# Kernel tuning notes

Measured on AMD Instinct MI355X. Metric: run time of the kernel, lower is better.

Reference implementation:

```python
import jax, jax.numpy as jnp
import numpy as np

C = 128   # recurrent/value channels
CK = 64   # key channels

def conv1x1(x, W, b):
    # x: [B,Cin,H,W], W: [Cout,Cin], b: [Cout]
    return jnp.einsum('bchw,oc->bohw', x, W) + b[None, :, None, None]

def extract_windows(x):
    # zero-padded 3x3 windows, matching F.unfold(kernel=3, padding=1)
    # x: [B,C,H2,W2] -> [B,C,9,H2,W2], tap order = (ky, kx) row-major
    B, c, H2, W2 = x.shape
    xp = jnp.pad(x, ((0, 0), (0, 0), (1, 1), (1, 1)))
    taps = [xp[:, :, dy:dy + H2, dx:dx + W2] for dy in range(3) for dx in range(3)]
    return jnp.stack(taps, axis=2)

def setup_inputs() -> dict:
    key = jax.random.key(0)
    ks = jax.random.split(key, 12)
    B, H, W = 2, 256, 512
    H2, W2 = 128, 256
    s = 0.02
    return {
        'h_prev': jax.random.normal(ks[0], (B, C, H2, W2), jnp.float32),
        'h_init': jax.random.normal(ks[1], (B, C, H, W), jnp.float32),
        'Wq':   jax.random.normal(ks[2], (CK, C), jnp.float32) * s,
        'bq':   jnp.zeros((CK,), jnp.float32),
        'Wk':   jax.random.normal(ks[3], (CK, C), jnp.float32) * s,
        'bk':   jnp.zeros((CK,), jnp.float32),
        'Wvp':  jax.random.normal(ks[4], (C, C), jnp.float32) * s,
        'bvp':  jnp.zeros((C,), jnp.float32),
        'Wvi':  jax.random.normal(ks[5], (C, C), jnp.float32) * s,
        'bvi':  jnp.zeros((C,), jnp.float32),
        'Wout': jax.random.normal(ks[6], (C, C), jnp.float32) * s,
        'bout': jnp.zeros((C,), jnp.float32),
    }

def reference(h_prev, h_init, Wq, bq, Wk, bk, Wvp, bvp, Wvi, bvi, Wout, bout):
    B, _, H, W = h_init.shape
    _, _, H2, W2 = h_prev.shape
    ry, rx = H // H2, W // W2

    q = conv1x1(h_init, Wq, bq)        # [B,CK,H,W]
    k = conv1x1(h_prev, Wk, bk)        # [B,CK,H2,W2]
    v = conv1x1(h_prev, Wvp, bvp)      # [B,C,H2,W2]

    k_win = extract_windows(k)         # [B,CK,9,H2,W2]
    v_win = extract_windows(v)         # [B,C,9,H2,W2]

    # q at fine res, grouped by coarse cell (nearest-neighbor broadcast of k/v)
    q_r = q.transpose(0, 2, 3, 1).reshape(B, H2, ry, W2, rx, CK)  # [B,H2,ry,W2,rx,CK]
    # scores over 9 window taps (zero-padded taps give score 0, as in unfold)
    scores = jnp.einsum('byaxdc,bcjyx->byaxdj', q_r, k_win)       # [B,H2,ry,W2,rx,9]
    a = jax.nn.softmax(scores, axis=-1)
    x = jnp.einsum('byaxdj,bcjyx->bcyaxd', a, v_win)              # [B,C,H2,ry,W2,rx]
    x = x.reshape(B, C, H, W)

    v_init = conv1x1(h_init, Wvi, bvi)
    return conv1x1(v_init + x, Wout, bout)
```

## Files before the change

### kernel.cpp

```cpp
#include <hip/hip_runtime.h>
#include <cstdint>
#include <cstddef>

#define THREADS 256
#define FTHREADS 512

typedef __attribute__((ext_vector_type(8))) short short8;
typedef __attribute__((ext_vector_type(4))) float f32x4;

#define MFMA(a, b, c) __builtin_amdgcn_mfma_f32_16x16x32_bf16((a), (b), (c), 0, 0, 0)

static constexpr int kC    = 128;
static constexpr int kImgC = 128 * 256;
static constexpr int kImgF = 256 * 512;

__device__ __forceinline__ unsigned short f2bf(float f) {
  unsigned u = __builtin_bit_cast(unsigned, f);
  u += 0x7fffu + ((u >> 16) & 1u);
  return (unsigned short)(u >> 16);
}
__device__ __forceinline__ unsigned pack_bf16(float lo, float hi) {
  return (unsigned)f2bf(lo) | ((unsigned)f2bf(hi) << 16);
}
__device__ __forceinline__ float bf_up(unsigned short u) {
  return __builtin_bit_cast(float, (unsigned)u << 16);
}

__device__ __forceinline__ void stage_tile(char* lds, const float* __restrict__ src,
                                           size_t cstride, int tid) {
  const int l = tid & 63, w = tid >> 6;
  const int pxl = l & 7;
  const int cg  = l >> 3;
  #pragma unroll
  for (int i = 0; i < 16; ++i) {
    const int px = pxl + 8 * (i & 7);
    const int c  = 2 * (cg + 8 * (w + 4 * (i >> 3)));
    float f0 = src[(size_t)c * cstride + px];
    float f1 = src[(size_t)(c + 1) * cstride + px];
    const int chunk = (c >> 3) ^ (px & 7);
    *(unsigned*)(lds + px * 256 + chunk * 16 + (c & 7) * 2) = pack_bf16(f0, f1);
  }
}

__device__ __forceinline__ short8 ldA(const char* lds, int mt, int kt, int l) {
  const int px = mt * 16 + (l & 15);
  const int chunk = (kt * 4 + (l >> 4)) ^ (px & 7);
  return *(const short8*)(lds + px * 256 + chunk * 16);
}

__global__ __launch_bounds__(THREADS) void cast_w(
    const float* __restrict__ Wq, const float* __restrict__ Wk,
    const float* __restrict__ Wvp, const float* __restrict__ Wvi,
    const float* __restrict__ Wout, unsigned short* __restrict__ dst) {
  int i = blockIdx.x * THREADS + threadIdx.x;
  float v;
  if (i < 8192)       v = Wq[i];
  else if (i < 16384) v = Wk[i - 8192];
  else if (i < 32768) v = Wvp[i - 16384];
  else if (i < 49152) v = Wvi[i - 32768];
  else                v = Wout[i - 49152];
  dst[i] = f2bf(v);
}

__global__ __launch_bounds__(THREADS, 4) void coarse_kv(
    const float* __restrict__ h_prev, const unsigned short* __restrict__ wbuf,
    const float* __restrict__ bk, const float* __restrict__ bvp,
    float* __restrict__ kbuf, float* __restrict__ vbuf) {
  __shared__ char xs[16384];
  const int tid = threadIdx.x;
  const int l = tid & 63, w = tid >> 6;
  const int m = l & 15, g = l >> 4;
  const int chq = w * 16 + m;

  const int tile = blockIdx.x;
  const int b    = tile >> 9;
  const int p0   = (tile & 511) * 64;
  const int p0g  = tile * 64;

  const short8* wkp = (const short8*)(wbuf + 8192);
  const short8* wvp = (const short8*)(wbuf + 16384);
  short8 fk[4], fv[2][4];
  #pragma unroll
  for (int kt = 0; kt < 4; ++kt) fk[kt] = wkp[chq * 16 + kt * 4 + g];
  #pragma unroll
  for (int nt = 0; nt < 2; ++nt)
    #pragma unroll
    for (int kt = 0; kt < 4; ++kt)
      fv[nt][kt] = wvp[(nt * 64 + chq) * 16 + kt * 4 + g];

  stage_tile(xs, h_prev + (size_t)b * kC * kImgC + p0, kImgC, tid);
  __syncthreads();

  {
    const float bl = bk[chq];
    #pragma unroll
    for (int mt = 0; mt < 4; ++mt) {
      f32x4 acc = {bl, bl, bl, bl};
      #pragma unroll
      for (int kt = 0; kt < 4; ++kt) acc = MFMA(ldA(xs, mt, kt, l), fk[kt], acc);
      #pragma unroll
      for (int r = 0; r < 4; ++r)
        kbuf[(size_t)(p0g + mt * 16 + g * 4 + r) * 64 + chq] = acc[r];
    }
  }
  #pragma unroll
  for (int nt = 0; nt < 2; ++nt) {
    const float bl = bvp[nt * 64 + chq];
    #pragma unroll
    for (int mt = 0; mt < 4; ++mt) {
      f32x4 acc = {bl, bl, bl, bl};
      #pragma unroll
      for (int kt = 0; kt < 4; ++kt) acc = MFMA(ldA(xs, mt, kt, l), fv[nt][kt], acc);
      #pragma unroll
      for (int r = 0; r < 4; ++r)
        vbuf[(size_t)(p0g + mt * 16 + g * 4 + r) * 128 + nt * 64 + chq] = acc[r];
    }
  }
}

__global__ __launch_bounds__(FTHREADS, 2) void fine_fused(
    const float* __restrict__ h_init, const unsigned short* __restrict__ wbuf,
    const float* __restrict__ bq, const float* __restrict__ bvi,
    const float* __restrict__ bout,
    const float* __restrict__ kbuf, const float* __restrict__ vbuf,
    float* __restrict__ out) {
  __shared__ char xs[32768];
  __shared__ unsigned short qs[128 * 72];
  __shared__ float ks_[102 * 76];
  __shared__ float vs_[102 * 140];

  const int tid = threadIdx.x;
  const int l = tid & 63, w = tid >> 6;
  const int m = l & 15, g = l >> 4;

  const int bid = blockIdx.x;
  const int b   = bid >> 10;
  const int r10 = bid & 1023;
  const int y2  = r10 >> 3;
  const int x0  = (r10 & 7) * 64;
  const int x20 = x0 >> 1;

  const size_t fbase = (size_t)b * kC * kImgF;
  const float* kb = kbuf + (size_t)b * kImgC * 64;
  const float* vb = vbuf + (size_t)b * kImgC * 128;

  const short8* wqp = (const short8*)wbuf;
  const short8* wip = (const short8*)(wbuf + 32768);
  const short8* wop = (const short8*)(wbuf + 49152);

  if (tid < 256)
    stage_tile(xs, h_init + fbase + (size_t)(2 * y2) * 512 + x0, kImgF, tid);
  else
    stage_tile(xs + 16384, h_init + fbase + (size_t)(2 * y2 + 1) * 512 + x0, kImgF, tid - 256);

  #pragma unroll
  for (int it = 0; it < 7; ++it) {
    const int i = tid + it * 512;
    if (i < 3264) {
      const int cy = i / 1088;
      const int rem = i - cy * 1088;
      const int cx = rem >> 5, cp = rem & 31;
      const int yy = y2 + cy - 1, xx = x20 + cx - 1;
      float2 kv = make_float2(0.f, 0.f);
      if (yy >= 0 && yy < 128 && xx >= 0 && xx < 256)
        kv = *(const float2*)(kb + ((size_t)yy * 256 + xx) * 64 + 2 * cp);
      *(float2*)(ks_ + (cy * 34 + cx) * 76 + 2 * cp) = kv;
    }
  }
  #pragma unroll
  for (int it = 0; it < 13; ++it) {
    const int i = tid + it * 512;
    if (i < 6528) {
      const int cy = i / 2176;
      const int rem = i - cy * 2176;
      const int cx = rem >> 6, cp = rem & 63;
      const int yy = y2 + cy - 1, xx = x20 + cx - 1;
      float2 vv = make_float2(0.f, 0.f);
      if (yy >= 0 && yy < 128 && xx >= 0 && xx < 256)
        vv = *(const float2*)(vb + ((size_t)yy * 256 + xx) * 128 + 2 * cp);
      *(float2*)(vs_ + (cy * 34 + cx) * 140 + 2 * cp) = vv;
    }
  }
  __syncthreads();

  const int chq4 = (w & 3) * 16 + m;
  const int hh   = w >> 2;
  {
    short8 fq[4];
    #pragma unroll
    for (int kt = 0; kt < 4; ++kt) fq[kt] = wqp[chq4 * 16 + kt * 4 + g];
    const float bl = bq[chq4];
    #pragma unroll
    for (int mt = 0; mt < 4; ++mt) {
      f32x4 acc = {bl, bl, bl, bl};
      #pragma unroll
      for (int kt = 0; kt < 4; ++kt) acc = MFMA(ldA(xs, hh * 4 + mt, kt, l), fq[kt], acc);
      #pragma unroll
      for (int r = 0; r < 4; ++r)
        qs[(hh * 64 + mt * 16 + g * 4 + r) * 72 + chq4] = f2bf(acc[r]);
    }
  }

  const int ch = w * 16 + m;
  f32x4 vacc[8];
  {
    short8 fi[4];
    #pragma unroll
    for (int kt = 0; kt < 4; ++kt) fi[kt] = wip[ch * 16 + kt * 4 + g];
    const float bl = bvi[ch];
    #pragma unroll
    for (int mt = 0; mt < 8; ++mt) {
      f32x4 acc = {bl, bl, bl, bl};
      #pragma unroll
      for (int kt = 0; kt < 4; ++kt) acc = MFMA(ldA(xs, mt, kt, l), fi[kt], acc);
      vacc[mt] = acc;
    }
  }
  __syncthreads();

  #pragma unroll
  for (int mt = 0; mt < 8; ++mt) {
    #pragma unroll
    for (int r = 0; r < 4; ++r) {
      const int px = mt * 16 + g * 4 + r;
      const int chunk = (ch >> 3) ^ (px & 7);
      *(unsigned short*)(xs + px * 256 + chunk * 16 + (ch & 7) * 2) = f2bf(vacc[mt][r]);
    }
  }
  __syncthreads();

  {
    const int apx = tid >> 2;
    const int sub = tid & 3;
    const int cc  = ((apx & 63) >> 1) + 1;

    float qf[16];
    {
      const uint4* qp = (const uint4*)((const char*)qs + apx * 144 + sub * 32);
      const uint4 u0 = qp[0], u1 = qp[1];
      const unsigned uu[8] = {u0.x, u0.y, u0.z, u0.w, u1.x, u1.y, u1.z, u1.w};
      #pragma unroll
      for (int i = 0; i < 8; ++i) {
        qf[2 * i]     = __builtin_bit_cast(float, uu[i] << 16);
        qf[2 * i + 1] = __builtin_bit_cast(float, uu[i] & 0xffff0000u);
      }
    }

    float a[9];
    #pragma unroll
    for (int j = 0; j < 9; ++j) {
      const int cell = (j / 3) * 34 + cc + (j % 3) - 1;
      const float4* kp = (const float4*)(ks_ + cell * 76 + sub * 16);
      const float4 k0 = kp[0], k1 = kp[1], k2 = kp[2], k3 = kp[3];
      float s = qf[0]*k0.x + qf[1]*k0.y + qf[2]*k0.z + qf[3]*k0.w
              + qf[4]*k1.x + qf[5]*k1.y + qf[6]*k1.z + qf[7]*k1.w
              + qf[8]*k2.x + qf[9]*k2.y + qf[10]*k2.z + qf[11]*k2.w
              + qf[12]*k3.x + qf[13]*k3.y + qf[14]*k3.z + qf[15]*k3.w;
      s += __shfl_xor(s, 1);
      s += __shfl_xor(s, 2);
      a[j] = s;
    }
    float mx = a[0];
    #pragma unroll
    for (int j = 1; j < 9; ++j) mx = fmaxf(mx, a[j]);
    float den = 0.f;
    #pragma unroll
    for (int j = 0; j < 9; ++j) { a[j] = __expf(a[j] - mx); den += a[j]; }
    const float inv = 1.f / den;

    float tt[32];
    #pragma unroll
    for (int i = 0; i < 32; ++i) tt[i] = 0.f;
    #pragma unroll
    for (int j = 0; j < 9; ++j) {
      const int cell = (j / 3) * 34 + cc + (j % 3) - 1;
      const float aj = a[j] * inv;
      const float4* vp = (const float4*)(vs_ + cell * 140 + sub * 32);
      const float4 v0 = vp[0], v1 = vp[1], v2 = vp[2], v3 = vp[3];
      const float4 v4 = vp[4], v5 = vp[5], v6 = vp[6], v7 = vp[7];
      tt[0]+=aj*v0.x;  tt[1]+=aj*v0.y;  tt[2]+=aj*v0.z;  tt[3]+=aj*v0.w;
      tt[4]+=aj*v1.x;  tt[5]+=aj*v1.y;  tt[6]+=aj*v1.z;  tt[7]+=aj*v1.w;
      tt[8]+=aj*v2.x;  tt[9]+=aj*v2.y;  tt[10]+=aj*v2.z; tt[11]+=aj*v2.w;
      tt[12]+=aj*v3.x; tt[13]+=aj*v3.y; tt[14]+=aj*v3.z; tt[15]+=aj*v3.w;
      tt[16]+=aj*v4.x; tt[17]+=aj*v4.y; tt[18]+=aj*v4.z; tt[19]+=aj*v4.w;
      tt[20]+=aj*v5.x; tt[21]+=aj*v5.y; tt[22]+=aj*v5.z; tt[23]+=aj*v5.w;
      tt[24]+=aj*v6.x; tt[25]+=aj*v6.y; tt[26]+=aj*v6.z; tt[27]+=aj*v6.w;
      tt[28]+=aj*v7.x; tt[29]+=aj*v7.y; tt[30]+=aj*v7.z; tt[31]+=aj*v7.w;
    }
    #pragma unroll
    for (int i = 0; i < 16; ++i) {
      const int c2 = sub * 32 + 2 * i;
      const int chunk = (c2 >> 3) ^ (apx & 7);
      unsigned* p = (unsigned*)(xs + apx * 256 + chunk * 16 + (c2 & 7) * 2);
      const unsigned u = *p;
      const float lo = bf_up((unsigned short)u) + tt[2 * i];
      const float hi = bf_up((unsigned short)(u >> 16)) + tt[2 * i + 1];
      *p = pack_bf16(lo, hi);
    }
  }
  __syncthreads();

  {
    short8 fo[4];
    #pragma unroll
    for (int kt = 0; kt < 4; ++kt) fo[kt] = wop[ch * 16 + kt * 4 + g];
    const float bl = bout[ch];
    #pragma unroll
    for (int mt = 0; mt < 8; ++mt) {
      f32x4 acc = {bl, bl, bl, bl};
      #pragma unroll
      for (int kt = 0; kt < 4; ++kt) acc = MFMA(ldA(xs, mt, kt, l), fo[kt], acc);
      const int px = mt * 16 + g * 4;
      *(float4*)(out + fbase + (size_t)ch * kImgF
                 + (size_t)(2 * y2 + (px >> 6)) * 512 + x0 + (px & 63)) =
          make_float4(acc[0], acc[1], acc[2], acc[3]);
    }
  }
}

extern "C" void kernel_launch(void* const* d_in, const int* in_sizes, int n_in,
                              void* d_out, int out_size, void* d_ws, size_t ws_size,
                              hipStream_t stream) {
  const float* h_prev = (const float*)d_in[0];
  const float* h_init = (const float*)d_in[1];
  const float* Wq   = (const float*)d_in[2];
  const float* bq   = (const float*)d_in[3];
  const float* Wk   = (const float*)d_in[4];
  const float* bk   = (const float*)d_in[5];
  const float* Wvp  = (const float*)d_in[6];
  const float* bvp  = (const float*)d_in[7];
  const float* Wvi  = (const float*)d_in[8];
  const float* bvi  = (const float*)d_in[9];
  const float* Wout = (const float*)d_in[10];
  const float* bout = (const float*)d_in[11];
  float* out = (float*)d_out;

  char* ws = (char*)d_ws;
  unsigned short* wbuf = (unsigned short*)ws;
  float* kbuf = (float*)(ws + 131072);
  float* vbuf = (float*)(ws + 131072 + (size_t)65536 * 64 * 4);

  cast_w<<<256, THREADS, 0, stream>>>(Wq, Wk, Wvp, Wvi, Wout, wbuf);
  coarse_kv<<<1024, THREADS, 0, stream>>>(h_prev, wbuf, bk, bvp, kbuf, vbuf);
  fine_fused<<<2048, FTHREADS, 0, stream>>>(h_init, wbuf, bq, bvi, bout,
                                            kbuf, vbuf, out);
}
```

Before: 394.1 us.

## Fuse coarse K/V projection into fine kernel, recomputing halo per block

Removes the separate coarse_kv kernel and its fp32 K/V workspace round-trip. Each fine block now loads the 3x34 coarse halo of h_prev, projects it to K and V with MFMA directly into shared memory, and zeroes out-of-bounds cells. The h_init tile is prefetched into registers before this work and written to LDS afterwards, so the global loads overlap the halo projection. The cost is redundant K/V computation, since each coarse cell is recomputed by several neighbouring blocks, plus higher register pressure from holding 32 prefetched floats per thread.

Result: slower. 436.3 us (+10.7%).

```diff
diff --git a/kernel.cpp b/kernel.cpp
--- a/kernel.cpp
+++ b/kernel.cpp
@@ -24,22 +24,6 @@
 }
 __device__ __forceinline__ float bf_up(unsigned short u) {
   return __builtin_bit_cast(float, (unsigned)u << 16);
-}
-
-__device__ __forceinline__ void stage_tile(char* lds, const float* __restrict__ src,
-                                           size_t cstride, int tid) {
-  const int l = tid & 63, w = tid >> 6;
-  const int pxl = l & 7;
-  const int cg  = l >> 3;
-  #pragma unroll
-  for (int i = 0; i < 16; ++i) {
-    const int px = pxl + 8 * (i & 7);
-    const int c  = 2 * (cg + 8 * (w + 4 * (i >> 3)));
-    float f0 = src[(size_t)c * cstride + px];
-    float f1 = src[(size_t)(c + 1) * cstride + px];
-    const int chunk = (c >> 3) ^ (px & 7);
-    *(unsigned*)(lds + px * 256 + chunk * 16 + (c & 7) * 2) = pack_bf16(f0, f1);
-  }
 }
 
 __device__ __forceinline__ short8 ldA(const char* lds, int mt, int kt, int l) {
@@ -62,68 +46,12 @@
   dst[i] = f2bf(v);
 }
 
-__global__ __launch_bounds__(THREADS, 4) void coarse_kv(
-    const float* __restrict__ h_prev, const unsigned short* __restrict__ wbuf,
-    const float* __restrict__ bk, const float* __restrict__ bvp,
-    float* __restrict__ kbuf, float* __restrict__ vbuf) {
-  __shared__ char xs[16384];
-  const int tid = threadIdx.x;
-  const int l = tid & 63, w = tid >> 6;
-  const int m = l & 15, g = l >> 4;
-  const int chq = w * 16 + m;
-
-  const int tile = blockIdx.x;
-  const int b    = tile >> 9;
-  const int p0   = (tile & 511) * 64;
-  const int p0g  = tile * 64;
-
-  const short8* wkp = (const short8*)(wbuf + 8192);
-  const short8* wvp = (const short8*)(wbuf + 16384);
-  short8 fk[4], fv[2][4];
-  #pragma unroll
-  for (int kt = 0; kt < 4; ++kt) fk[kt] = wkp[chq * 16 + kt * 4 + g];
-  #pragma unroll
-  for (int nt = 0; nt < 2; ++nt)
-    #pragma unroll
-    for (int kt = 0; kt < 4; ++kt)
-      fv[nt][kt] = wvp[(nt * 64 + chq) * 16 + kt * 4 + g];
-
-  stage_tile(xs, h_prev + (size_t)b * kC * kImgC + p0, kImgC, tid);
-  __syncthreads();
-
-  {
-    const float bl = bk[chq];
-    #pragma unroll
-    for (int mt = 0; mt < 4; ++mt) {
-      f32x4 acc = {bl, bl, bl, bl};
-      #pragma unroll
-      for (int kt = 0; kt < 4; ++kt) acc = MFMA(ldA(xs, mt, kt, l), fk[kt], acc);
-      #pragma unroll
-      for (int r = 0; r < 4; ++r)
-        kbuf[(size_t)(p0g + mt * 16 + g * 4 + r) * 64 + chq] = acc[r];
-    }
-  }
-  #pragma unroll
-  for (int nt = 0; nt < 2; ++nt) {
-    const float bl = bvp[nt * 64 + chq];
-    #pragma unroll
-    for (int mt = 0; mt < 4; ++mt) {
-      f32x4 acc = {bl, bl, bl, bl};
-      #pragma unroll
-      for (int kt = 0; kt < 4; ++kt) acc = MFMA(ldA(xs, mt, kt, l), fv[nt][kt], acc);
-      #pragma unroll
-      for (int r = 0; r < 4; ++r)
-        vbuf[(size_t)(p0g + mt * 16 + g * 4 + r) * 128 + nt * 64 + chq] = acc[r];
-    }
-  }
-}
-
 __global__ __launch_bounds__(FTHREADS, 2) void fine_fused(
-    const float* __restrict__ h_init, const unsigned short* __restrict__ wbuf,
-    const float* __restrict__ bq, const float* __restrict__ bvi,
-    const float* __restrict__ bout,
-    const float* __restrict__ kbuf, const float* __restrict__ vbuf,
-    float* __restrict__ out) {
+    const float* __restrict__ h_prev, const float* __restrict__ h_init,
+    const unsigned short* __restrict__ wbuf,
+    const float* __restrict__ bq, const float* __restrict__ bk,
+    const float* __restrict__ bvp, const float* __restrict__ bvi,
+    const float* __restrict__ bout, float* __restrict__ out) {
   __shared__ char xs[32768];
   __shared__ unsigned short qs[128 * 72];
   __shared__ float ks_[102 * 76];
@@ -141,44 +69,83 @@
   const int x20 = x0 >> 1;
 
   const size_t fbase = (size_t)b * kC * kImgF;
-  const float* kb = kbuf + (size_t)b * kImgC * 64;
-  const float* vb = vbuf + (size_t)b * kImgC * 128;
 
   const short8* wqp = (const short8*)wbuf;
+  const short8* wkp = (const short8*)(wbuf + 8192);
+  const short8* wvp = (const short8*)(wbuf + 16384);
   const short8* wip = (const short8*)(wbuf + 32768);
   const short8* wop = (const short8*)(wbuf + 49152);
 
-  if (tid < 256)
-    stage_tile(xs, h_init + fbase + (size_t)(2 * y2) * 512 + x0, kImgF, tid);
-  else
-    stage_tile(xs + 16384, h_init + fbase + (size_t)(2 * y2 + 1) * 512 + x0, kImgF, tid - 256);
-
+  const int tl = tid & 255;
+  const int sl = tl & 63, sw = tl >> 6;
+  const int spxl = sl & 7, scg = sl >> 3;
+  const float* xsrc = h_init + fbase + (size_t)(2 * y2 + (tid >> 8)) * 512 + x0;
+  float xf0[16], xf1[16];
   #pragma unroll
-  for (int it = 0; it < 7; ++it) {
-    const int i = tid + it * 512;
-    if (i < 3264) {
-      const int cy = i / 1088;
-      const int rem = i - cy * 1088;
-      const int cx = rem >> 5, cp = rem & 31;
+  for (int i = 0; i < 16; ++i) {
+    const int px = spxl + 8 * (i & 7);
+    const int c  = 2 * (scg + 8 * (sw + 4 * (i >> 3)));
+    xf0[i] = xsrc[(size_t)c * kImgF + px];
+    xf1[i] = xsrc[(size_t)(c + 1) * kImgF + px];
+  }
+
+  {
+    const float* hp = h_prev + (size_t)b * kC * kImgC;
+    const int pxl = l & 7, cg8 = l >> 3;
+    const int c = 2 * (cg8 + 8 * w);
+    #pragma unroll
+    for (int t = 0; t < 13; ++t) {
+      const int p = pxl + 8 * t;
+      const int cy = p / 34, cx = p - cy * 34;
       const int yy = y2 + cy - 1, xx = x20 + cx - 1;
-      float2 kv = make_float2(0.f, 0.f);
-      if (yy >= 0 && yy < 128 && xx >= 0 && xx < 256)
-        kv = *(const float2*)(kb + ((size_t)yy * 256 + xx) * 64 + 2 * cp);
-      *(float2*)(ks_ + (cy * 34 + cx) * 76 + 2 * cp) = kv;
-    }
-  }
-  #pragma unroll
-  for (int it = 0; it < 13; ++it) {
-    const int i = tid + it * 512;
-    if (i < 6528) {
-      const int cy = i / 2176;
-      const int rem = i - cy * 2176;
-      const int cx = rem >> 6, cp = rem & 63;
-      const int yy = y2 + cy - 1, xx = x20 + cx - 1;
-      float2 vv = make_float2(0.f, 0.f);
-      if (yy >= 0 && yy < 128 && xx >= 0 && xx < 256)
-        vv = *(const float2*)(vb + ((size_t)yy * 256 + xx) * 128 + 2 * cp);
-      *(float2*)(vs_ + (cy * 34 + cx) * 140 + 2 * cp) = vv;
+      float f0 = 0.f, f1 = 0.f;
+      if (p < 102 && (unsigned)yy < 128u && (unsigned)xx < 256u) {
+        const size_t pos = (size_t)yy * 256 + xx;
+        f0 = hp[(size_t)c * kImgC + pos];
+        f1 = hp[(size_t)(c + 1) * kImgC + pos];
+      }
+      if (p < 102) {
+        const int chunk = (c >> 3) ^ (p & 7);
+        *(unsigned*)(xs + p * 256 + chunk * 16 + (c & 7) * 2) = pack_bf16(f0, f1);
+      }
+    }
+  }
+  __syncthreads();
+
+  for (int j = w; j < 84; j += 8) {
+    const int mt = j / 12, cg12 = j - mt * 12;
+    const bool isk = cg12 < 4;
+    const int och = (isk ? cg12 : cg12 - 4) * 16 + m;
+    const short8* wp = isk ? wkp : wvp;
+    const float bl = isk ? bk[och] : bvp[och];
+    f32x4 acc = {bl, bl, bl, bl};
+    #pragma unroll
+    for (int kt = 0; kt < 4; ++kt)
+      acc = MFMA(ldA(xs, mt, kt, l), wp[och * 16 + kt * 4 + g], acc);
+    #pragma unroll
+    for (int r = 0; r < 4; ++r) {
+      const int cell = mt * 16 + g * 4 + r;
+      if (cell < 102) {
+        const int cy = cell / 34, cx = cell - cy * 34;
+        const int yy = y2 + cy - 1, xx = x20 + cx - 1;
+        const float val =
+            ((unsigned)yy < 128u && (unsigned)xx < 256u) ? acc[r] : 0.f;
+        if (isk) ks_[cell * 76 + och] = val;
+        else     vs_[cell * 140 + och] = val;
+      }
+    }
+  }
+  __syncthreads();
+
+  {
+    char* dst = xs + (tid >> 8) * 16384;
+    #pragma unroll
+    for (int i = 0; i < 16; ++i) {
+      const int px = spxl + 8 * (i & 7);
+      const int c  = 2 * (scg + 8 * (sw + 4 * (i >> 3)));
+      const int chunk = (c >> 3) ^ (px & 7);
+      *(unsigned*)(dst + px * 256 + chunk * 16 + (c & 7) * 2) =
+          pack_bf16(xf0[i], xf1[i]);
     }
   }
   __syncthreads();
@@ -337,11 +304,8 @@
 
   char* ws = (char*)d_ws;
   unsigned short* wbuf = (unsigned short*)ws;
-  float* kbuf = (float*)(ws + 131072);
-  float* vbuf = (float*)(ws + 131072 + (size_t)65536 * 64 * 4);
 
   cast_w<<<256, THREADS, 0, stream>>>(Wq, Wk, Wvp, Wvi, Wout, wbuf);
-  coarse_kv<<<1024, THREADS, 0, stream>>>(h_prev, wbuf, bk, bvp, kbuf, vbuf);
-  fine_fused<<<2048, FTHREADS, 0, stream>>>(h_init, wbuf, bq, bvi, bout,
-                                            kbuf, vbuf, out);
-}
+  fine_fused<<<2048, FTHREADS, 0, stream>>>(h_prev, h_init, wbuf,
+                                            bq, bk, bvp, bvi, bout, out);
+}
```

## Store K/V in bf16 and tile fine kernel as 8x16 2D blocks

Applied to the files above, without the earlier changes.

Coarse K and V intermediates are now written as bf16 instead of fp32, halving their global traffic and LDS footprint. The fine kernel switches from 2-row by 64-column tiles to 8-row by 16-column tiles, so the coarse halo shrinks from 3x34 cells to 6x10 cells per block, which cuts redundant K/V staging. Smaller LDS use allows launch bounds of 4 blocks per CU. The tradeoffs are extra bf16 rounding of K/V and narrower 64-byte row segments in global loads and stores.

Measured after the change: 369.0 us. -6.4%, faster.

```diff
diff --git a/kernel.cpp b/kernel.cpp
--- a/kernel.cpp
+++ b/kernel.cpp
@@ -25,21 +25,11 @@
 __device__ __forceinline__ float bf_up(unsigned short u) {
   return __builtin_bit_cast(float, (unsigned)u << 16);
 }
-
-__device__ __forceinline__ void stage_tile(char* lds, const float* __restrict__ src,
-                                           size_t cstride, int tid) {
-  const int l = tid & 63, w = tid >> 6;
-  const int pxl = l & 7;
-  const int cg  = l >> 3;
-  #pragma unroll
-  for (int i = 0; i < 16; ++i) {
-    const int px = pxl + 8 * (i & 7);
-    const int c  = 2 * (cg + 8 * (w + 4 * (i >> 3)));
-    float f0 = src[(size_t)c * cstride + px];
-    float f1 = src[(size_t)(c + 1) * cstride + px];
-    const int chunk = (c >> 3) ^ (px & 7);
-    *(unsigned*)(lds + px * 256 + chunk * 16 + (c & 7) * 2) = pack_bf16(f0, f1);
-  }
+__device__ __forceinline__ float bf_lo(unsigned u) {
+  return __builtin_bit_cast(float, u << 16);
+}
+__device__ __forceinline__ float bf_hi(unsigned u) {
+  return __builtin_bit_cast(float, u & 0xffff0000u);
 }
 
 __device__ __forceinline__ short8 ldA(const char* lds, int mt, int kt, int l) {
@@ -65,7 +55,7 @@
 __global__ __launch_bounds__(THREADS, 4) void coarse_kv(
     const float* __restrict__ h_prev, const unsigned short* __restrict__ wbuf,
     const float* __restrict__ bk, const float* __restrict__ bvp,
-    float* __restrict__ kbuf, float* __restrict__ vbuf) {
+    unsigned short* __restrict__ kbuf, unsigned short* __restrict__ vbuf) {
   __shared__ char xs[16384];
   const int tid = threadIdx.x;
   const int l = tid & 63, w = tid >> 6;
@@ -88,7 +78,19 @@
     for (int kt = 0; kt < 4; ++kt)
       fv[nt][kt] = wvp[(nt * 64 + chq) * 16 + kt * 4 + g];
 
-  stage_tile(xs, h_prev + (size_t)b * kC * kImgC + p0, kImgC, tid);
+  {
+    const float* src = h_prev + (size_t)b * kC * kImgC + p0;
+    const int pxl = l & 7, cg = l >> 3;
+    #pragma unroll
+    for (int i = 0; i < 16; ++i) {
+      const int px = pxl + 8 * (i & 7);
+      const int c  = 2 * (cg + 8 * (w + 4 * (i >> 3)));
+      float f0 = src[(size_t)c * kImgC + px];
+      float f1 = src[(size_t)(c + 1) * kImgC + px];
+      const int chunk = (c >> 3) ^ (px & 7);
+      *(unsigned*)(xs + px * 256 + chunk * 16 + (c & 7) * 2) = pack_bf16(f0, f1);
+    }
+  }
   __syncthreads();
 
   {
@@ -100,7 +102,7 @@
       for (int kt = 0; kt < 4; ++kt) acc = MFMA(ldA(xs, mt, kt, l), fk[kt], acc);
       #pragma unroll
       for (int r = 0; r < 4; ++r)
-        kbuf[(size_t)(p0g + mt * 16 + g * 4 + r) * 64 + chq] = acc[r];
+        kbuf[(size_t)(p0g + mt * 16 + g * 4 + r) * 64 + chq] = f2bf(acc[r]);
     }
   }
   #pragma unroll
@@ -113,21 +115,21 @@
       for (int kt = 0; kt < 4; ++kt) acc = MFMA(ldA(xs, mt, kt, l), fv[nt][kt], acc);
       #pragma unroll
       for (int r = 0; r < 4; ++r)
-        vbuf[(size_t)(p0g + mt * 16 + g * 4 + r) * 128 + nt * 64 + chq] = acc[r];
-    }
-  }
-}
-
-__global__ __launch_bounds__(FTHREADS, 2) void fine_fused(
+        vbuf[(size_t)(p0g + mt * 16 + g * 4 + r) * 128 + nt * 64 + chq] = f2bf(acc[r]);
+    }
+  }
+}
+
+__global__ __launch_bounds__(FTHREADS, 4) void fine_fused(
     const float* __restrict__ h_init, const unsigned short* __restrict__ wbuf,
     const float* __restrict__ bq, const float* __restrict__ bvi,
     const float* __restrict__ bout,
-    const float* __restrict__ kbuf, const float* __restrict__ vbuf,
+    const unsigned short* __restrict__ kbuf, const unsigned short* __restrict__ vbuf,
     float* __restrict__ out) {
   __shared__ char xs[32768];
   __shared__ unsigned short qs[128 * 72];
-  __shared__ float ks_[102 * 76];
-  __shared__ float vs_[102 * 140];
+  __shared__ unsigned short ks_[60 * 80];
+  __shared__ unsigned short vs_[60 * 144];
 
   const int tid = threadIdx.x;
   const int l = tid & 63, w = tid >> 6;
@@ -136,49 +138,63 @@
   const int bid = blockIdx.x;
   const int b   = bid >> 10;
   const int r10 = bid & 1023;
-  const int y2  = r10 >> 3;
-  const int x0  = (r10 & 7) * 64;
+  const int ty  = r10 >> 5;
+  const int tx  = r10 & 31;
+  const int y0  = ty * 8;
+  const int x0  = tx * 16;
+  const int y20 = y0 >> 1;
   const int x20 = x0 >> 1;
 
   const size_t fbase = (size_t)b * kC * kImgF;
-  const float* kb = kbuf + (size_t)b * kImgC * 64;
-  const float* vb = vbuf + (size_t)b * kImgC * 128;
+  const unsigned short* kb = kbuf + (size_t)b * kImgC * 64;
+  const unsigned short* vb = vbuf + (size_t)b * kImgC * 128;
 
   const short8* wqp = (const short8*)wbuf;
   const short8* wip = (const short8*)(wbuf + 32768);
   const short8* wop = (const short8*)(wbuf + 49152);
 
-  if (tid < 256)
-    stage_tile(xs, h_init + fbase + (size_t)(2 * y2) * 512 + x0, kImgF, tid);
-  else
-    stage_tile(xs + 16384, h_init + fbase + (size_t)(2 * y2 + 1) * 512 + x0, kImgF, tid - 256);
-
-  #pragma unroll
-  for (int it = 0; it < 7; ++it) {
+  {
+    const int half = tid >> 8;
+    const int tl = tid & 255;
+    const int sl = tl & 63, sw = tl >> 6;
+    const int pxl = sl & 7, cg = sl >> 3;
+    #pragma unroll
+    for (int i = 0; i < 16; ++i) {
+      const int px = half * 64 + pxl + 8 * (i & 7);
+      const int row = px >> 4, col = px & 15;
+      const int c  = 2 * (cg + 8 * (sw + 4 * (i >> 3)));
+      const size_t off = (size_t)(y0 + row) * 512 + x0 + col;
+      float f0 = h_init[fbase + (size_t)c * kImgF + off];
+      float f1 = h_init[fbase + (size_t)(c + 1) * kImgF + off];
+      const int chunk = (c >> 3) ^ (px & 7);
+      *(unsigned*)(xs + px * 256 + chunk * 16 + (c & 7) * 2) = pack_bf16(f0, f1);
+    }
+  }
+
+  #pragma unroll
+  for (int it = 0; it < 2; ++it) {
     const int i = tid + it * 512;
-    if (i < 3264) {
-      const int cy = i / 1088;
-      const int rem = i - cy * 1088;
-      const int cx = rem >> 5, cp = rem & 31;
-      const int yy = y2 + cy - 1, xx = x20 + cx - 1;
-      float2 kv = make_float2(0.f, 0.f);
-      if (yy >= 0 && yy < 128 && xx >= 0 && xx < 256)
-        kv = *(const float2*)(kb + ((size_t)yy * 256 + xx) * 64 + 2 * cp);
-      *(float2*)(ks_ + (cy * 34 + cx) * 76 + 2 * cp) = kv;
-    }
-  }
-  #pragma unroll
-  for (int it = 0; it < 13; ++it) {
+    if (i < 960) {
+      const int cell = i >> 4, cp = i & 15;
+      const int cy = cell / 10, cx = cell - cy * 10;
+      const int yy = y20 + cy - 1, xx = x20 + cx - 1;
+      uint2 val = make_uint2(0u, 0u);
+      if ((unsigned)yy < 128u && (unsigned)xx < 256u)
+        val = *(const uint2*)(kb + ((size_t)yy * 256 + xx) * 64 + cp * 4);
+      *(uint2*)((char*)ks_ + cell * 160 + (cp >> 2) * 40 + (cp & 3) * 8) = val;
+    }
+  }
+  #pragma unroll
+  for (int it = 0; it < 4; ++it) {
     const int i = tid + it * 512;
-    if (i < 6528) {
-      const int cy = i / 2176;
-      const int rem = i - cy * 2176;
-      const int cx = rem >> 6, cp = rem & 63;
-      const int yy = y2 + cy - 1, xx = x20 + cx - 1;
-      float2 vv = make_float2(0.f, 0.f);
-      if (yy >= 0 && yy < 128 && xx >= 0 && xx < 256)
-        vv = *(const float2*)(vb + ((size_t)yy * 256 + xx) * 128 + 2 * cp);
-      *(float2*)(vs_ + (cy * 34 + cx) * 140 + 2 * cp) = vv;
+    if (i < 1920) {
+      const int cell = i >> 5, cp = i & 31;
+      const int cy = cell / 10, cx = cell - cy * 10;
+      const int yy = y20 + cy - 1, xx = x20 + cx - 1;
+      uint2 val = make_uint2(0u, 0u);
+      if ((unsigned)yy < 128u && (unsigned)xx < 256u)
+        val = *(const uint2*)(vb + ((size_t)yy * 256 + xx) * 128 + cp * 4);
+      *(uint2*)((char*)vs_ + cell * 288 + (cp >> 3) * 72 + (cp & 7) * 8) = val;
     }
   }
   __syncthreads();
@@ -232,7 +248,8 @@
   {
     const int apx = tid >> 2;
     const int sub = tid & 3;
-    const int cc  = ((apx & 63) >> 1) + 1;
+    const int r2  = apx >> 5;
+    const int c2  = (apx & 15) >> 1;
 
     float qf[16];
     {
@@ -241,21 +258,25 @@
       const unsigned uu[8] = {u0.x, u0.y, u0.z, u0.w, u1.x, u1.y, u1.z, u1.w};
       #pragma unroll
       for (int i = 0; i < 8; ++i) {
-        qf[2 * i]     = __builtin_bit_cast(float, uu[i] << 16);
-        qf[2 * i + 1] = __builtin_bit_cast(float, uu[i] & 0xffff0000u);
+        qf[2 * i]     = bf_lo(uu[i]);
+        qf[2 * i + 1] = bf_hi(uu[i]);
       }
     }
 
     float a[9];
     #pragma unroll
     for (int j = 0; j < 9; ++j) {
-      const int cell = (j / 3) * 34 + cc + (j % 3) - 1;
-      const float4* kp = (const float4*)(ks_ + cell * 76 + sub * 16);
-      const float4 k0 = kp[0], k1 = kp[1], k2 = kp[2], k3 = kp[3];
-      float s = qf[0]*k0.x + qf[1]*k0.y + qf[2]*k0.z + qf[3]*k0.w
-              + qf[4]*k1.x + qf[5]*k1.y + qf[6]*k1.z + qf[7]*k1.w
-              + qf[8]*k2.x + qf[9]*k2.y + qf[10]*k2.z + qf[11]*k2.w
-              + qf[12]*k3.x + qf[13]*k3.y + qf[14]*k3.z + qf[15]*k3.w;
+      const int cell = (r2 + j / 3) * 10 + c2 + (j % 3);
+      const char* kc = (const char*)ks_ + cell * 160 + sub * 40;
+      const uint2 u0 = *(const uint2*)kc;
+      const uint2 u1 = *(const uint2*)(kc + 8);
+      const uint2 u2 = *(const uint2*)(kc + 16);
+      const uint2 u3 = *(const uint2*)(kc + 24);
+      const unsigned uu[8] = {u0.x, u0.y, u1.x, u1.y, u2.x, u2.y, u3.x, u3.y};
+      float s = 0.f;
+      #pragma unroll
+      for (int i = 0; i < 8; ++i)
+        s += qf[2 * i] * bf_lo(uu[i]) + qf[2 * i + 1] * bf_hi(uu[i]);
       s += __shfl_xor(s, 1);
       s += __shfl_xor(s, 2);
       a[j] = s;
@@ -273,27 +294,25 @@
     for (int i = 0; i < 32; ++i) tt[i] = 0.f;
     #pragma unroll
     for (int j = 0; j < 9; ++j) {
-      const int cell = (j / 3) * 34 + cc + (j % 3) - 1;
+      const int cell = (r2 + j / 3) * 10 + c2 + (j % 3);
       const float aj = a[j] * inv;
-      const float4* vp = (const float4*)(vs_ + cell * 140 + sub * 32);
-      const float4 v0 = vp[0], v1 = vp[1], v2 = vp[2], v3 = vp[3];
-      const float4 v4 = vp[4], v5 = vp[5], v6 = vp[6], v7 = vp[7];
-      tt[0]+=aj*v0.x;  tt[1]+=aj*v0.y;  tt[2]+=aj*v0.z;  tt[3]+=aj*v0.w;
-      tt[4]+=aj*v1.x;  tt[5]+=aj*v1.y;  tt[6]+=aj*v1.z;  tt[7]+=aj*v1.w;
-      tt[8]+=aj*v2.x;  tt[9]+=aj*v2.y;  tt[10]+=aj*v2.z; tt[11]+=aj*v2.w;
-      tt[12]+=aj*v3.x; tt[13]+=aj*v3.y; tt[14]+=aj*v3.z; tt[15]+=aj*v3.w;
-      tt[16]+=aj*v4.x; tt[17]+=aj*v4.y; tt[18]+=aj*v4.z; tt[19]+=aj*v4.w;
-      tt[20]+=aj*v5.x; tt[21]+=aj*v5.y; tt[22]+=aj*v5.z; tt[23]+=aj*v5.w;
-      tt[24]+=aj*v6.x; tt[25]+=aj*v6.y; tt[26]+=aj*v6.z; tt[27]+=aj*v6.w;
-      tt[28]+=aj*v7.x; tt[29]+=aj*v7.y; tt[30]+=aj*v7.z; tt[31]+=aj*v7.w;
+      const char* vc = (const char*)vs_ + cell * 288 + sub * 72;
+      #pragma unroll
+      for (int q2 = 0; q2 < 8; ++q2) {
+        const uint2 u = *(const uint2*)(vc + q2 * 8);
+        tt[4 * q2]     += aj * bf_lo(u.x);
+        tt[4 * q2 + 1] += aj * bf_hi(u.x);
+        tt[4 * q2 + 2] += aj * bf_lo(u.y);
+        tt[4 * q2 + 3] += aj * bf_hi(u.y);
+      }
     }
     #pragma unroll
     for (int i = 0; i < 16; ++i) {
-      const int c2 = sub * 32 + 2 * i;
-      const int chunk = (c2 >> 3) ^ (apx & 7);
-      unsigned* p = (unsigned*)(xs + apx * 256 + chunk * 16 + (c2 & 7) * 2);
+      const int cc2 = sub * 32 + 2 * i;
+      const int chunk = (cc2 >> 3) ^ (apx & 7);
+      unsigned* p = (unsigned*)(xs + apx * 256 + chunk * 16 + (cc2 & 7) * 2);
       const unsigned u = *p;
-      const float lo = bf_up((unsigned short)u) + tt[2 * i];
+      const float lo = bf_lo(u) + tt[2 * i];
       const float hi = bf_up((unsigned short)(u >> 16)) + tt[2 * i + 1];
       *p = pack_bf16(lo, hi);
     }
@@ -310,9 +329,8 @@
       f32x4 acc = {bl, bl, bl, bl};
       #pragma unroll
       for (int kt = 0; kt < 4; ++kt) acc = MFMA(ldA(xs, mt, kt, l), fo[kt], acc);
-      const int px = mt * 16 + g * 4;
       *(float4*)(out + fbase + (size_t)ch * kImgF
-                 + (size_t)(2 * y2 + (px >> 6)) * 512 + x0 + (px & 63)) =
+                 + (size_t)(y0 + mt) * 512 + x0 + g * 4) =
           make_float4(acc[0], acc[1], acc[2], acc[3]);
     }
   }
@@ -337,8 +355,8 @@
 
   char* ws = (char*)d_ws;
   unsigned short* wbuf = (unsigned short*)ws;
-  float* kbuf = (float*)(ws + 131072);
-  float* vbuf = (float*)(ws + 131072 + (size_t)65536 * 64 * 4);
+  unsigned short* kbuf = (unsigned short*)(ws + 131072);
+  unsigned short* vbuf = (unsigned short*)(ws + 131072 + (size_t)65536 * 64 * 2);
 
   cast_w<<<256, THREADS, 0, stream>>>(Wq, Wk, Wvp, Wvi, Wout, wbuf);
   coarse_kv<<<1024, THREADS, 0, stream>>>(h_prev, wbuf, bk, bvp, kbuf, vbuf);
```
